# Optimization experiments

Hardware: AMD Instinct MI355X
Metric: run time of the kernel (lower is better)

The kernel has to match this reference:

```python
import jax, jax.numpy as jnp
import numpy as np


def mlp(x, W1, b1, W2, b2):
    # x: [D] -> y: [O]
    return jnp.tanh(x @ W1 + b1) @ W2 + b2


def christoffel(x, W1, b1, W2, b2):
    """Per-example Christoffel symbols Gamma[k,i,j] for one point x: [D].

    Faithful to the torch code: the 'metric' used for Gamma is built from
    gradients of the FIRST n_dims outputs (y_flat[:, i], i < n_dims), i.e.
    G = Jn Jn^T with Jn the jacobian restricted to the first D outputs.
    """
    D = x.shape[-1]
    f = lambda z: mlp(z, W1, b1, W2, b2)[:D]          # first D outputs

    def metric(z):
        J = jax.jacrev(f)(z)                           # [D, D]
        return J @ J.T                                 # G[i,j] = grad_i . grad_j

    dG = jax.jacfwd(metric)(x)                         # dG[i,j,k] = dG_ij/dx_k
    # Gamma[k,i,j] = 0.5 * (dG[i,j,k] + dG[i,k,j] - dG[j,k,i])
    return 0.5 * (dG.transpose((2, 0, 1)) + dG.transpose((1, 0, 2)) - dG.transpose((1, 2, 0)))


def setup_inputs() -> dict:
    key = jax.random.key(0)
    k1, k2, k3, k4, k5 = jax.random.split(key, 5)
    B, D, H, O = 32, 64, 2048, 64
    return {
        "x0": jnp.zeros((B, D), jnp.float32),
        "xT": jax.random.normal(k1, (B, D), jnp.float32),
        "W1": jax.random.normal(k2, (D, H), jnp.float32) / np.sqrt(D),
        "b1": jax.random.normal(k3, (H,), jnp.float32) * 0.02,
        "W2": jax.random.normal(k4, (H, O), jnp.float32) / np.sqrt(H),
        "b2": jax.random.normal(k5, (O,), jnp.float32) * 0.02,
        "n_steps": 10,
    }


def reference(x0, xT, W1, b1, W2, b2, n_steps):
    B, D = x0.shape
    t = jnp.linspace(0.0, 1.0, n_steps)                    # [S]
    # straight-line interpolation paths  [S, B, D]
    straight = x0[None] + t[:, None, None] * (xT - x0)[None]
    v = xT - x0
    v = v / jnp.linalg.norm(v, axis=1, keepdims=True)      # [B, D]

    interior = straight[1:-1].reshape(-1, D)               # [(S-2)*B, D]
    Gamma = jax.vmap(christoffel, in_axes=(0, None, None, None, None))(
        interior, W1, b1, W2, b2
    ).reshape(n_steps - 2, B, D, D, D)                     # [S-2, B, k, i, j]

    # correction[b,mu] = -sum_{k,i} Gamma[b,k,i,mu] v[b,k] v[b,i]
    corr = -jnp.einsum('sbkim,bk,bi->sbm', Gamma, v, v)    # [S-2, B, D]
    t_int = t[1:-1]
    t_factor = (t_int * (1.0 - t_int))[:, None, None]
    scale = jnp.minimum(jnp.linalg.norm(corr, axis=2, keepdims=True), 0.1)
    corr = corr * t_factor * scale * 0.1

    paths = straight.at[1:-1].add(corr)                    # [S, B, D]
    return paths.reshape(-1, D)                            # [S*B, D]
```

## Files before the change

### kernel.cpp

```cpp
#include <hip/hip_runtime.h>
#include <math.h>


#define D64 64

typedef float floatx2 __attribute__((ext_vector_type(2)));

__device__ __forceinline__ floatx2 fp8_lo(unsigned u) {
    return __builtin_amdgcn_cvt_pk_f32_fp8(u, false);
}
__device__ __forceinline__ floatx2 fp8_hi(unsigned u) {
    return __builtin_amdgcn_cvt_pk_f32_fp8(u, true);
}
__device__ __forceinline__ unsigned char f2fp8(float x) {
    return (unsigned char)(__builtin_amdgcn_cvt_pk_fp8_f32(x, 0.f, 0, false) & 0xFF);
}

__global__ __launch_bounds__(256) void k_prep(
    const float* __restrict__ x0, const float* __restrict__ xT,
    const float* __restrict__ W1, const float* __restrict__ b1,
    const float* __restrict__ W2,
    unsigned char* __restrict__ W1q,
    float* __restrict__ Z0, float* __restrict__ Zd, float* __restrict__ C,
    float* __restrict__ out, int B, int H, int n_steps)
{
    const int b   = blockIdx.y;
    const int tid = threadIdx.x;
    const int h   = blockIdx.x * 256 + tid;

    __shared__ float x0L[D64], dL[D64], vL[D64];
    if (tid < D64) {
        const float a0 = x0[b * D64 + tid];
        const float aT = xT[b * D64 + tid];
        const float d  = aT - a0;
        float ss = d * d;
        #pragma unroll
        for (int off = 32; off; off >>= 1) ss += __shfl_xor(ss, off);
        const float inv = 1.0f / sqrtf(ss);
        x0L[tid] = a0; dL[tid] = d; vL[tid] = d * inv;
        if (blockIdx.x == 0) {
            out[(size_t)(0 * B + b) * D64 + tid]             = a0;
            out[(size_t)((n_steps - 1) * B + b) * D64 + tid] = aT;
        }
    }
    __syncthreads();

    float z0 = b1[h];
    float zd = 0.f;
    if (b == 0) {
        #pragma unroll
        for (int d = 0; d < D64; ++d) {
            const float w = W1[(size_t)d * H + h];
            W1q[(size_t)d * H + h] = f2fp8(w);
            z0 = fmaf(x0L[d], w, z0);
            zd = fmaf(dL[d],  w, zd);
        }
    } else {
        #pragma unroll
        for (int d = 0; d < D64; ++d) {
            const float w = W1[(size_t)d * H + h];
            z0 = fmaf(x0L[d], w, z0);
            zd = fmaf(dL[d],  w, zd);
        }
    }

    float c = 0.f;
    const float4* w2r = reinterpret_cast<const float4*>(W2 + (size_t)h * D64);
    #pragma unroll
    for (int i = 0; i < D64 / 4; ++i) {
        const float4 w = w2r[i];
        c = fmaf(w.x, vL[4*i],     c);
        c = fmaf(w.y, vL[4*i + 1], c);
        c = fmaf(w.z, vL[4*i + 2], c);
        c = fmaf(w.w, vL[4*i + 3], c);
    }

    Z0[(size_t)b * H + h] = z0;
    Zd[(size_t)b * H + h] = zd;
    C [(size_t)b * H + h] = c;
}

__global__ __launch_bounds__(1024) void k_fused(
    const float* __restrict__ x0, const float* __restrict__ xT,
    const unsigned char* __restrict__ W1q,
    const float* __restrict__ Z0, const float* __restrict__ Zd,
    const float* __restrict__ C,
    float* __restrict__ out, int B, int H, int n_steps)
{
    const int n    = blockIdx.x;
    const int s8   = n / B;
    const int b    = n % B;
    const int tid  = threadIdx.x;
    const int lane = tid & 63;
    const int wv   = tid >> 6;

    __shared__ float pL[2048];
    __shared__ float qL[2048];
    __shared__ float gradL[D64];
    __shared__ float corrL[D64];

    const float ts = (float)(s8 + 1) / (float)(n_steps - 1);

    {
        const float2 z0 = reinterpret_cast<const float2*>(Z0 + (size_t)b * H)[tid];
        const float2 zd = reinterpret_cast<const float2*>(Zd + (size_t)b * H)[tid];
        const float2 c  = reinterpret_cast<const float2*>(C  + (size_t)b * H)[tid];
        const float zx = fmaf(ts, zd.x, z0.x);
        const float zy = fmaf(ts, zd.y, z0.y);
        const float tx = tanhf(zx), ty = tanhf(zy);
        const float sx = 1.f - tx * tx, sy = 1.f - ty * ty;
        pL[2 * tid]     = c.x * sx;
        pL[2 * tid + 1] = c.y * sy;
        qL[2 * tid]     = -2.f * c.x * tx * sx;
        qL[2 * tid + 1] = -2.f * c.y * ty * sy;
    }
    __syncthreads();

    #pragma unroll
    for (int rr = 0; rr < 4; ++rr) {
        const int a = wv * 4 + rr;
        const unsigned* wrow = reinterpret_cast<const unsigned*>(W1q + (size_t)a * H);
        float acc = 0.f;
        #pragma unroll
        for (int j = 0; j < 8; ++j) {
            const unsigned w  = wrow[lane + j * 64];
            const float4   p  = reinterpret_cast<const float4*>(pL)[lane + j * 64];
            const floatx2  w0 = fp8_lo(w);
            const floatx2  w1 = fp8_hi(w);
            acc = fmaf(w0.x, p.x, acc);
            acc = fmaf(w0.y, p.y, acc);
            acc = fmaf(w1.x, p.z, acc);
            acc = fmaf(w1.y, p.w, acc);
        }
        #pragma unroll
        for (int off = 32; off; off >>= 1) acc += __shfl_xor(acc, off);
        if (lane == 0) gradL[a] = acc;
    }
    __syncthreads();

    {
        float2 r = make_float2(0.f, 0.f);
        #pragma unroll 16
        for (int d = 0; d < D64; ++d) {
            const unsigned w = *reinterpret_cast<const unsigned short*>(
                                   W1q + (size_t)d * H + 2 * tid);
            const floatx2 wf = fp8_lo(w);
            const float    g = gradL[d];
            r.x = fmaf(g, wf.x, r.x);
            r.y = fmaf(g, wf.y, r.y);
        }
        pL[2 * tid]     = qL[2 * tid]     * r.x;
        pL[2 * tid + 1] = qL[2 * tid + 1] * r.y;
    }
    __syncthreads();

    #pragma unroll
    for (int rr = 0; rr < 4; ++rr) {
        const int a = wv * 4 + rr;
        const unsigned* wrow = reinterpret_cast<const unsigned*>(W1q + (size_t)a * H);
        float acc = 0.f;
        #pragma unroll
        for (int j = 0; j < 8; ++j) {
            const unsigned w  = wrow[lane + j * 64];
            const float4   p  = reinterpret_cast<const float4*>(pL)[lane + j * 64];
            const floatx2  w0 = fp8_lo(w);
            const floatx2  w1 = fp8_hi(w);
            acc = fmaf(w0.x, p.x, acc);
            acc = fmaf(w0.y, p.y, acc);
            acc = fmaf(w1.x, p.z, acc);
            acc = fmaf(w1.y, p.w, acc);
        }
        #pragma unroll
        for (int off = 32; off; off >>= 1) acc += __shfl_xor(acc, off);
        if (lane == 0) corrL[a] = -acc;
    }
    __syncthreads();

    if (tid < D64) {
        const float a0 = x0[b * D64 + tid];
        const float aT = xT[b * D64 + tid];
        const float d  = aT - a0;
        const float cm = corrL[tid];
        float n2 = cm * cm;
        #pragma unroll
        for (int off = 32; off; off >>= 1) n2 += __shfl_xor(n2, off);
        const float scale  = fminf(sqrtf(n2), 0.1f);
        const float factor = ts * (1.f - ts) * scale * 0.1f;
        out[(size_t)((s8 + 1) * B + b) * D64 + tid] = fmaf(cm, factor, fmaf(ts, d, a0));
    }
}

extern "C" void kernel_launch(void* const* d_in, const int* in_sizes, int n_in,
                              void* d_out, int out_size, void* d_ws, size_t ws_size,
                              hipStream_t stream) {
    const float* x0 = (const float*)d_in[0];
    const float* xT = (const float*)d_in[1];
    const float* W1 = (const float*)d_in[2];
    const float* b1 = (const float*)d_in[3];
    const float* W2 = (const float*)d_in[4];
    float* out = (float*)d_out;

    const int H       = in_sizes[3];
    const int D       = in_sizes[2] / H;
    const int B       = in_sizes[0] / D;
    const int n_steps = out_size / (B * D);
    const int NI      = n_steps - 2;
    const int NP      = NI * B;

    unsigned char* W1q = (unsigned char*)d_ws;
    float* Z0 = (float*)(W1q + (size_t)D * H);
    float* Zd = Z0 + (size_t)B * H;
    float* C  = Zd + (size_t)B * H;

    k_prep<<<dim3(H / 256, B), dim3(256), 0, stream>>>(
        x0, xT, W1, b1, W2, W1q, Z0, Zd, C, out, B, H, n_steps);
    k_fused<<<dim3(NP), dim3(1024), 0, stream>>>(
        x0, xT, W1q, Z0, Zd, C, out, B, H, n_steps);
}
```

Before: 79.92 us.

## Fuse prep and Christoffel kernels into one launch with flag-based inter-block sync

Merges the precompute kernel (tanh preactivations, W2·v projections, FP8 quantization of W1) into the main per-point kernel. Each block first produces one chunk of prep data, then publishes it with a release-store of a magic flag. Consumer blocks spin on the flags for their batch row and the W1q chunks before running the gradient passes, and fall back to recomputing the missing data themselves after a timeout. This removes one kernel launch and the boundary between the two kernels, at the cost of spin-waiting and a dependence on all blocks being resident together. The flags are never reset, so later calls may see stale flags and read buffers while they are being rewritten.

```diff
diff --git a/kernel.cpp b/kernel.cpp
--- a/kernel.cpp
+++ b/kernel.cpp
@@ -2,7 +2,9 @@
 #include <math.h>
 
 
-#define D64 64
+#define D64   64
+#define CHUNK 256
+#define MAGIC 0x3C96A5E1u
 
 typedef float floatx2 __attribute__((ext_vector_type(2)));
 
@@ -16,90 +18,163 @@
     return (unsigned char)(__builtin_amdgcn_cvt_pk_fp8_f32(x, 0.f, 0, false) & 0xFF);
 }
 
-__global__ __launch_bounds__(256) void k_prep(
+__global__ __launch_bounds__(1024) void k_geo(
     const float* __restrict__ x0, const float* __restrict__ xT,
     const float* __restrict__ W1, const float* __restrict__ b1,
     const float* __restrict__ W2,
     unsigned char* __restrict__ W1q,
     float* __restrict__ Z0, float* __restrict__ Zd, float* __restrict__ C,
-    float* __restrict__ out, int B, int H, int n_steps)
-{
-    const int b   = blockIdx.y;
-    const int tid = threadIdx.x;
-    const int h   = blockIdx.x * 256 + tid;
-
-    __shared__ float x0L[D64], dL[D64], vL[D64];
-    if (tid < D64) {
-        const float a0 = x0[b * D64 + tid];
-        const float aT = xT[b * D64 + tid];
-        const float d  = aT - a0;
-        float ss = d * d;
-        #pragma unroll
-        for (int off = 32; off; off >>= 1) ss += __shfl_xor(ss, off);
-        const float inv = 1.0f / sqrtf(ss);
-        x0L[tid] = a0; dL[tid] = d; vL[tid] = d * inv;
-        if (blockIdx.x == 0) {
-            out[(size_t)(0 * B + b) * D64 + tid]             = a0;
-            out[(size_t)((n_steps - 1) * B + b) * D64 + tid] = aT;
-        }
-    }
-    __syncthreads();
-
-    float z0 = b1[h];
-    float zd = 0.f;
-    if (b == 0) {
-        #pragma unroll
-        for (int d = 0; d < D64; ++d) {
-            const float w = W1[(size_t)d * H + h];
-            W1q[(size_t)d * H + h] = f2fp8(w);
-            z0 = fmaf(x0L[d], w, z0);
-            zd = fmaf(dL[d],  w, zd);
-        }
-    } else {
-        #pragma unroll
-        for (int d = 0; d < D64; ++d) {
-            const float w = W1[(size_t)d * H + h];
-            z0 = fmaf(x0L[d], w, z0);
-            zd = fmaf(dL[d],  w, zd);
-        }
-    }
-
-    float c = 0.f;
-    const float4* w2r = reinterpret_cast<const float4*>(W2 + (size_t)h * D64);
-    #pragma unroll
-    for (int i = 0; i < D64 / 4; ++i) {
-        const float4 w = w2r[i];
-        c = fmaf(w.x, vL[4*i],     c);
-        c = fmaf(w.y, vL[4*i + 1], c);
-        c = fmaf(w.z, vL[4*i + 2], c);
-        c = fmaf(w.w, vL[4*i + 3], c);
-    }
-
-    Z0[(size_t)b * H + h] = z0;
-    Zd[(size_t)b * H + h] = zd;
-    C [(size_t)b * H + h] = c;
-}
-
-__global__ __launch_bounds__(1024) void k_fused(
-    const float* __restrict__ x0, const float* __restrict__ xT,
-    const unsigned char* __restrict__ W1q,
-    const float* __restrict__ Z0, const float* __restrict__ Zd,
-    const float* __restrict__ C,
+    unsigned int* __restrict__ flags,
     float* __restrict__ out, int B, int H, int n_steps)
 {
     const int n    = blockIdx.x;
-    const int s8   = n / B;
-    const int b    = n % B;
     const int tid  = threadIdx.x;
     const int lane = tid & 63;
     const int wv   = tid >> 6;
-
+    const int NCH  = H / CHUNK;
+
+    __shared__ float x0L[D64], dL[D64], vL[D64];
     __shared__ float pL[2048];
     __shared__ float qL[2048];
     __shared__ float gradL[D64];
     __shared__ float corrL[D64];
-
+    __shared__ unsigned int missL;
+
+    const int b_p = n / NCH;
+    const int hx  = n % NCH;
+    if (b_p < B) {
+        if (tid < D64) {
+            const float a0 = x0[b_p * D64 + tid];
+            const float aT = xT[b_p * D64 + tid];
+            const float d  = aT - a0;
+            float ss = d * d;
+            #pragma unroll
+            for (int off = 32; off; off >>= 1) ss += __shfl_xor(ss, off);
+            const float inv = 1.0f / sqrtf(ss);
+            x0L[tid] = a0; dL[tid] = d; vL[tid] = d * inv;
+        }
+        __syncthreads();
+        if (tid < CHUNK) {
+            const int h = hx * CHUNK + tid;
+            float z0 = b1[h];
+            float zd = 0.f;
+            if (b_p == 0) {
+                #pragma unroll 8
+                for (int d = 0; d < D64; ++d) {
+                    const float w = W1[(size_t)d * H + h];
+                    W1q[(size_t)d * H + h] = f2fp8(w);
+                    z0 = fmaf(x0L[d], w, z0);
+                    zd = fmaf(dL[d],  w, zd);
+                }
+            } else {
+                #pragma unroll 8
+                for (int d = 0; d < D64; ++d) {
+                    const float w = W1[(size_t)d * H + h];
+                    z0 = fmaf(x0L[d], w, z0);
+                    zd = fmaf(dL[d],  w, zd);
+                }
+            }
+            float c = 0.f;
+            const float4* w2r = reinterpret_cast<const float4*>(W2 + (size_t)h * D64);
+            #pragma unroll
+            for (int i = 0; i < D64 / 4; ++i) {
+                const float4 w = w2r[i];
+                c = fmaf(w.x, vL[4*i],     c);
+                c = fmaf(w.y, vL[4*i + 1], c);
+                c = fmaf(w.z, vL[4*i + 2], c);
+                c = fmaf(w.w, vL[4*i + 3], c);
+            }
+            Z0[(size_t)b_p * H + h] = z0;
+            Zd[(size_t)b_p * H + h] = zd;
+            C [(size_t)b_p * H + h] = c;
+        }
+        __syncthreads();
+        if (tid == 0) {
+            __hip_atomic_store(&flags[b_p * NCH + hx], MAGIC,
+                               __ATOMIC_RELEASE, __HIP_MEMORY_SCOPE_AGENT);
+            if (b_p == 0)
+                __hip_atomic_store(&flags[B * NCH + hx], MAGIC,
+                                   __ATOMIC_RELEASE, __HIP_MEMORY_SCOPE_AGENT);
+        }
+    }
+
+    const int s8 = n / B;
+    const int b  = n % B;
     const float ts = (float)(s8 + 1) / (float)(n_steps - 1);
+
+    if (s8 == 0 && tid < D64) {
+        const float a0 = x0[b * D64 + tid];
+        const float aT = xT[b * D64 + tid];
+        out[(size_t)(0 * B + b) * D64 + tid]             = a0;
+        out[(size_t)((n_steps - 1) * B + b) * D64 + tid] = aT;
+    }
+
+    if (wv == 0) {
+        const bool need = lane < 2 * NCH;
+        unsigned int* addr = need
+            ? (lane < NCH ? &flags[b * NCH + lane] : &flags[B * NCH + (lane - NCH)])
+            : &flags[0];
+        bool ok = !need;
+        int iter = 0;
+        while (true) {
+            if (!ok) ok = (__hip_atomic_load(addr, __ATOMIC_RELAXED,
+                                             __HIP_MEMORY_SCOPE_AGENT) == MAGIC);
+            if (__all(ok)) { if (lane == 0) missL = 0u; break; }
+            if (++iter > 60000) {
+                const unsigned long long bal = __ballot(ok);
+                if (lane == 0) missL = (unsigned)(~bal) & 0xFFFFu;
+                break;
+            }
+            __builtin_amdgcn_s_sleep(2);
+        }
+        if (need && ok)
+            (void)__hip_atomic_load(addr, __ATOMIC_ACQUIRE, __HIP_MEMORY_SCOPE_AGENT);
+    }
+    __syncthreads();
+    const unsigned miss = missL;
+    if (miss) {
+        if (tid < D64) {
+            const float a0 = x0[b * D64 + tid];
+            const float aT = xT[b * D64 + tid];
+            const float d  = aT - a0;
+            float ss = d * d;
+            #pragma unroll
+            for (int off = 32; off; off >>= 1) ss += __shfl_xor(ss, off);
+            const float inv = 1.0f / sqrtf(ss);
+            x0L[tid] = a0; dL[tid] = d; vL[tid] = d * inv;
+        }
+        __syncthreads();
+        for (int k = 0; k < NCH; ++k) {
+            if ((miss & (1u << k)) && tid < CHUNK) {
+                const int h = k * CHUNK + tid;
+                float z0 = b1[h], zd = 0.f;
+                #pragma unroll 8
+                for (int d = 0; d < D64; ++d) {
+                    const float w = W1[(size_t)d * H + h];
+                    z0 = fmaf(x0L[d], w, z0);
+                    zd = fmaf(dL[d],  w, zd);
+                }
+                float c = 0.f;
+                const float4* w2r = reinterpret_cast<const float4*>(W2 + (size_t)h * D64);
+                #pragma unroll
+                for (int i = 0; i < D64 / 4; ++i) {
+                    const float4 w = w2r[i];
+                    c = fmaf(w.x, vL[4*i],   c); c = fmaf(w.y, vL[4*i+1], c);
+                    c = fmaf(w.z, vL[4*i+2], c); c = fmaf(w.w, vL[4*i+3], c);
+                }
+                Z0[(size_t)b * H + h] = z0;
+                Zd[(size_t)b * H + h] = zd;
+                C [(size_t)b * H + h] = c;
+            }
+            if ((miss & (1u << (NCH + k))) && tid < CHUNK) {
+                const int h = k * CHUNK + tid;
+                #pragma unroll 8
+                for (int d = 0; d < D64; ++d)
+                    W1q[(size_t)d * H + h] = f2fp8(W1[(size_t)d * H + h]);
+            }
+        }
+        __syncthreads();
+    }
 
     {
         const float2 z0 = reinterpret_cast<const float2*>(Z0 + (size_t)b * H)[tid];
@@ -211,9 +286,8 @@
     float* Z0 = (float*)(W1q + (size_t)D * H);
     float* Zd = Z0 + (size_t)B * H;
     float* C  = Zd + (size_t)B * H;
-
-    k_prep<<<dim3(H / 256, B), dim3(256), 0, stream>>>(
-        x0, xT, W1, b1, W2, W1q, Z0, Zd, C, out, B, H, n_steps);
-    k_fused<<<dim3(NP), dim3(1024), 0, stream>>>(
-        x0, xT, W1q, Z0, Zd, C, out, B, H, n_steps);
-}
+    unsigned int* flags = (unsigned int*)(C + (size_t)B * H);
+
+    k_geo<<<dim3(NP), dim3(1024), 0, stream>>>(
+        x0, xT, W1, b1, W2, W1q, Z0, Zd, C, flags, out, B, H, n_steps);
+}
```

New measurement: 87.61 us. 9.6% more time.

## Stage fp8 W1 in LDS via direct loads, split prep reduction, pack FMAs

Applied to the files above, without the earlier changes.

The fused kernel now copies the whole 128KB fp8 W1 matrix into shared memory with global_load_lds at the start of each block, and all three matvec passes read it from LDS instead of global memory. The prep kernel splits the D-reduction across two halves of a 512-thread block and combines the partial sums through shared memory to increase parallelism. The inner loops use packed two-wide float FMAs. The cost is 128KB of LDS per block, which limits occupancy to one block per CU. There is no explicit wait on the asynchronous LDS load before it is read, apart from the existing __syncthreads.

```diff
diff --git a/kernel.cpp b/kernel.cpp
--- a/kernel.cpp
+++ b/kernel.cpp
@@ -16,7 +16,7 @@
     return (unsigned char)(__builtin_amdgcn_cvt_pk_fp8_f32(x, 0.f, 0, false) & 0xFF);
 }
 
-__global__ __launch_bounds__(256) void k_prep(
+__global__ __launch_bounds__(512) void k_prep(
     const float* __restrict__ x0, const float* __restrict__ xT,
     const float* __restrict__ W1, const float* __restrict__ b1,
     const float* __restrict__ W2,
@@ -24,11 +24,15 @@
     float* __restrict__ Z0, float* __restrict__ Zd, float* __restrict__ C,
     float* __restrict__ out, int B, int H, int n_steps)
 {
-    const int b   = blockIdx.y;
-    const int tid = threadIdx.x;
-    const int h   = blockIdx.x * 256 + tid;
+    const int b    = blockIdx.y;
+    const int tid  = threadIdx.x;
+    const int t8   = tid & 255;
+    const int half = tid >> 8;
+    const int h    = blockIdx.x * 256 + t8;
 
     __shared__ float x0L[D64], dL[D64], vL[D64];
+    __shared__ float pz0[256], pzd[256], pc[256];
+
     if (tid < D64) {
         const float a0 = x0[b * D64 + tid];
         const float aT = xT[b * D64 + tid];
@@ -45,11 +49,12 @@
     }
     __syncthreads();
 
-    float z0 = b1[h];
+    const int d0 = half * 32;
+    float z0 = half ? 0.f : b1[h];
     float zd = 0.f;
     if (b == 0) {
         #pragma unroll
-        for (int d = 0; d < D64; ++d) {
+        for (int d = d0; d < d0 + 32; ++d) {
             const float w = W1[(size_t)d * H + h];
             W1q[(size_t)d * H + h] = f2fp8(w);
             z0 = fmaf(x0L[d], w, z0);
@@ -57,7 +62,7 @@
         }
     } else {
         #pragma unroll
-        for (int d = 0; d < D64; ++d) {
+        for (int d = d0; d < d0 + 32; ++d) {
             const float w = W1[(size_t)d * H + h];
             z0 = fmaf(x0L[d], w, z0);
             zd = fmaf(dL[d],  w, zd);
@@ -65,19 +70,23 @@
     }
 
     float c = 0.f;
-    const float4* w2r = reinterpret_cast<const float4*>(W2 + (size_t)h * D64);
-    #pragma unroll
-    for (int i = 0; i < D64 / 4; ++i) {
+    const float4* w2r = reinterpret_cast<const float4*>(W2 + (size_t)h * D64 + d0);
+    #pragma unroll
+    for (int i = 0; i < 8; ++i) {
         const float4 w = w2r[i];
-        c = fmaf(w.x, vL[4*i],     c);
-        c = fmaf(w.y, vL[4*i + 1], c);
-        c = fmaf(w.z, vL[4*i + 2], c);
-        c = fmaf(w.w, vL[4*i + 3], c);
-    }
-
-    Z0[(size_t)b * H + h] = z0;
-    Zd[(size_t)b * H + h] = zd;
-    C [(size_t)b * H + h] = c;
+        c = fmaf(w.x, vL[d0 + 4*i],     c);
+        c = fmaf(w.y, vL[d0 + 4*i + 1], c);
+        c = fmaf(w.z, vL[d0 + 4*i + 2], c);
+        c = fmaf(w.w, vL[d0 + 4*i + 3], c);
+    }
+
+    if (half) { pz0[t8] = z0; pzd[t8] = zd; pc[t8] = c; }
+    __syncthreads();
+    if (!half) {
+        Z0[(size_t)b * H + h] = z0 + pz0[t8];
+        Zd[(size_t)b * H + h] = zd + pzd[t8];
+        C [(size_t)b * H + h] = c  + pc[t8];
+    }
 }
 
 __global__ __launch_bounds__(1024) void k_fused(
@@ -94,12 +103,22 @@
     const int lane = tid & 63;
     const int wv   = tid >> 6;
 
+    __shared__ unsigned char w1s[D64 * 2048];
     __shared__ float pL[2048];
     __shared__ float qL[2048];
     __shared__ float gradL[D64];
     __shared__ float corrL[D64];
 
     const float ts = (float)(s8 + 1) / (float)(n_steps - 1);
+
+    #pragma unroll
+    for (int j = 0; j < 8; ++j) {
+        const int loff = j * 16384 + wv * 1024;
+        __builtin_amdgcn_global_load_lds(
+            (const __attribute__((address_space(1))) void*)(W1q + loff + lane * 16),
+            (__attribute__((address_space(3))) void*)(w1s + loff),
+            16, 0, 0);
+    }
 
     {
         const float2 z0 = reinterpret_cast<const float2*>(Z0 + (size_t)b * H)[tid];
@@ -119,19 +138,20 @@
     #pragma unroll
     for (int rr = 0; rr < 4; ++rr) {
         const int a = wv * 4 + rr;
-        const unsigned* wrow = reinterpret_cast<const unsigned*>(W1q + (size_t)a * H);
-        float acc = 0.f;
+        const unsigned* wrow = reinterpret_cast<const unsigned*>(w1s + a * 2048);
+        floatx2 acc2 = {0.f, 0.f};
         #pragma unroll
         for (int j = 0; j < 8; ++j) {
             const unsigned w  = wrow[lane + j * 64];
             const float4   p  = reinterpret_cast<const float4*>(pL)[lane + j * 64];
             const floatx2  w0 = fp8_lo(w);
             const floatx2  w1 = fp8_hi(w);
-            acc = fmaf(w0.x, p.x, acc);
-            acc = fmaf(w0.y, p.y, acc);
-            acc = fmaf(w1.x, p.z, acc);
-            acc = fmaf(w1.y, p.w, acc);
-        }
+            floatx2 p01; p01.x = p.x; p01.y = p.y;
+            floatx2 p23; p23.x = p.z; p23.y = p.w;
+            acc2 = w0 * p01 + acc2;
+            acc2 = w1 * p23 + acc2;
+        }
+        float acc = acc2.x + acc2.y;
         #pragma unroll
         for (int off = 32; off; off >>= 1) acc += __shfl_xor(acc, off);
         if (lane == 0) gradL[a] = acc;
@@ -139,37 +159,38 @@
     __syncthreads();
 
     {
-        float2 r = make_float2(0.f, 0.f);
+        floatx2 r2 = {0.f, 0.f};
         #pragma unroll 16
         for (int d = 0; d < D64; ++d) {
-            const unsigned w = *reinterpret_cast<const unsigned short*>(
-                                   W1q + (size_t)d * H + 2 * tid);
-            const floatx2 wf = fp8_lo(w);
+            const unsigned short ws = *reinterpret_cast<const unsigned short*>(
+                                          w1s + d * 2048 + 2 * tid);
+            const floatx2 wf = fp8_lo((unsigned)ws);
             const float    g = gradL[d];
-            r.x = fmaf(g, wf.x, r.x);
-            r.y = fmaf(g, wf.y, r.y);
-        }
-        pL[2 * tid]     = qL[2 * tid]     * r.x;
-        pL[2 * tid + 1] = qL[2 * tid + 1] * r.y;
+            floatx2 g2; g2.x = g; g2.y = g;
+            r2 = wf * g2 + r2;
+        }
+        pL[2 * tid]     = qL[2 * tid]     * r2.x;
+        pL[2 * tid + 1] = qL[2 * tid + 1] * r2.y;
     }
     __syncthreads();
 
     #pragma unroll
     for (int rr = 0; rr < 4; ++rr) {
         const int a = wv * 4 + rr;
-        const unsigned* wrow = reinterpret_cast<const unsigned*>(W1q + (size_t)a * H);
-        float acc = 0.f;
+        const unsigned* wrow = reinterpret_cast<const unsigned*>(w1s + a * 2048);
+        floatx2 acc2 = {0.f, 0.f};
         #pragma unroll
         for (int j = 0; j < 8; ++j) {
             const unsigned w  = wrow[lane + j * 64];
             const float4   p  = reinterpret_cast<const float4*>(pL)[lane + j * 64];
             const floatx2  w0 = fp8_lo(w);
             const floatx2  w1 = fp8_hi(w);
-            acc = fmaf(w0.x, p.x, acc);
-            acc = fmaf(w0.y, p.y, acc);
-            acc = fmaf(w1.x, p.z, acc);
-            acc = fmaf(w1.y, p.w, acc);
-        }
+            floatx2 p01; p01.x = p.x; p01.y = p.y;
+            floatx2 p23; p23.x = p.z; p23.y = p.w;
+            acc2 = w0 * p01 + acc2;
+            acc2 = w1 * p23 + acc2;
+        }
+        float acc = acc2.x + acc2.y;
         #pragma unroll
         for (int off = 32; off; off >>= 1) acc += __shfl_xor(acc, off);
         if (lane == 0) corrL[a] = -acc;
@@ -212,7 +233,7 @@
     float* Zd = Z0 + (size_t)B * H;
     float* C  = Zd + (size_t)B * H;
 
-    k_prep<<<dim3(H / 256, B), dim3(256), 0, stream>>>(
+    k_prep<<<dim3(H / 256, B), dim3(512), 0, stream>>>(
         x0, xT, W1, b1, W2, W1q, Z0, Zd, C, out, B, H, n_steps);
     k_fused<<<dim3(NP), dim3(1024), 0, stream>>>(
         x0, xT, W1q, Z0, Zd, C, out, B, H, n_steps);
```

Measured after the change: 81.03 us. No clear change (+1.4%).
